# Kernel tuning notes

Hardware: AMD Instinct MI355X
Metric: run time of the kernel (lower is better)

The kernel has to match this reference:

```python
import jax, jax.numpy as jnp
import numpy as np

N = 65536      # total nodes = B * MAXN
E = 524288     # edges (avg degree 8)
DX = 32; DG = 32
IN_DIM = DX + 3 * DG   # 128, after concat(x, g0, g1, g2)
H = 256; OUT = 8; MAXN = 8192


def setup_inputs() -> dict:
    key = jax.random.key(0)
    ks = jax.random.split(key, 40)
    inp = {}
    inp['x'] = jax.random.normal(ks[0], (N, DX), jnp.float32)
    inp['g0'] = jax.random.normal(ks[1], (N, DG), jnp.float32)
    inp['g1'] = jax.random.normal(ks[2], (N, DG), jnp.float32)
    inp['g2'] = jax.random.normal(ks[3], (N, DG), jnp.float32)
    inp['edge_src'] = jax.random.randint(ks[4], (E,), 0, N, jnp.int32)
    inp['edge_dst'] = jax.random.randint(ks[5], (E,), 0, N, jnp.int32)
    dims = [(IN_DIM, H), (H, H), (H, H), (H, H)]
    k = 6
    for i, (di, do) in enumerate(dims):
        s = 1.0 / np.sqrt(di)
        inp[f'Wl{i}'] = jax.random.uniform(ks[k], (di, do), jnp.float32, -s, s); k += 1
        inp[f'Wr{i}'] = jax.random.uniform(ks[k], (di, do), jnp.float32, -s, s); k += 1
        inp[f'b{i}'] = jnp.zeros((do,), jnp.float32)
    s = 1.0 / np.sqrt(MAXN)
    inp['mlp1_W1'] = jax.random.uniform(ks[k], (MAXN, H), jnp.float32, -s, s); k += 1
    inp['mlp1_b1'] = jnp.zeros((H,), jnp.float32)
    s = 1.0 / np.sqrt(H)
    inp['mlp1_W2'] = jax.random.uniform(ks[k], (H, 1), jnp.float32, -s, s); k += 1
    inp['mlp1_b2'] = jnp.zeros((1,), jnp.float32)
    inp['bn_gamma'] = jnp.ones((H,), jnp.float32)
    inp['bn_beta'] = jnp.zeros((H,), jnp.float32)
    inp['mlp2_W1'] = jax.random.uniform(ks[k], (H, H), jnp.float32, -s, s); k += 1
    inp['mlp2_b1'] = jnp.zeros((H,), jnp.float32)
    inp['mlp2_W2'] = jax.random.uniform(ks[k], (H, OUT), jnp.float32, -s, s); k += 1
    inp['mlp2_b2'] = jnp.zeros((OUT,), jnp.float32)
    return inp


def _forward(x, g0, g1, g2, edge_src, edge_dst,
             Wl0, Wr0, b0, Wl1, Wr1, b1, Wl2, Wr2, b2, Wl3, Wr3, b3,
             mlp1_W1, mlp1_b1, mlp1_W2, mlp1_b2, bn_gamma, bn_beta,
             mlp2_W1, mlp2_b1, mlp2_W2, mlp2_b2):
    h = jnp.concatenate([x, g0, g1, g2], axis=1)  # [N, IN_DIM]
    # mean-aggregation denominator (in-degree, clamped at 1 like PyG mean)
    cnt = jnp.maximum(
        jax.ops.segment_sum(jnp.ones((E,), h.dtype), edge_dst, num_segments=N), 1.0)
    for Wl, Wr, b in ((Wl0, Wr0, b0), (Wl1, Wr1, b1), (Wl2, Wr2, b2), (Wl3, Wr3, b3)):
        agg = jax.ops.segment_sum(h[edge_src], edge_dst, num_segments=N) / cnt[:, None]
        # SAGEConv: lin_l(mean of neighbors) + lin_r(self) + bias, then ReLU
        h = jax.nn.relu(agg @ Wl + h @ Wr + b)
        # F.dropout in eval / deterministic reference: identity
    h = h.reshape(-1, H, MAXN)                               # [B, H, MAXN]
    h = jax.nn.relu(jnp.einsum('bhm,mk->bhk', h, mlp1_W1) + mlp1_b1)
    h = (jnp.einsum('bhk,ko->bho', h, mlp1_W2) + mlp1_b2)[..., 0]  # [B, H]
    mean = h.mean(axis=0)
    var = h.var(axis=0)
    h = (h - mean) / jnp.sqrt(var + 1e-5) * bn_gamma + bn_beta
    h = jax.nn.relu(h)
    h = jax.nn.relu(h @ mlp2_W1 + mlp2_b1)
    return h @ mlp2_W2 + mlp2_b2                              # [B, OUT]


def reference(x, g0, g1, g2, edge_src, edge_dst,
              Wl0, Wr0, b0, Wl1, Wr1, b1, Wl2, Wr2, b2, Wl3, Wr3, b3,
              mlp1_W1, mlp1_b1, mlp1_W2, mlp1_b2, bn_gamma, bn_beta,
              mlp2_W1, mlp2_b1, mlp2_W2, mlp2_b2):
    return _forward(x, g0, g1, g2, edge_src, edge_dst,
                    Wl0, Wr0, b0, Wl1, Wr1, b1, Wl2, Wr2, b2, Wl3, Wr3, b3,
                    mlp1_W1, mlp1_b1, mlp1_W2, mlp1_b2, bn_gamma, bn_beta,
                    mlp2_W1, mlp2_b1, mlp2_W2, mlp2_b2)
```

## Files before the change

### kernel.cpp

```cpp
#include <hip/hip_runtime.h>
#include <hip/hip_bf16.h>


#define NN 65536
#define EE 524288
#define ROWS 65537
#define PCSR_CAP 983040

using frag16 = __attribute__((ext_vector_type(8))) short;
using f32x4  = __attribute__((ext_vector_type(4))) float;
using us8    = __attribute__((ext_vector_type(8))) unsigned short;
using us4v   = __attribute__((ext_vector_type(4))) unsigned short;

__device__ __forceinline__ float b2f(unsigned short u) {
    union { unsigned u32; float f; } x; x.u32 = (unsigned)u << 16; return x.f;
}

__device__ __forceinline__ void gld_lds16(const void* g, void* l) {
    __builtin_amdgcn_global_load_lds(
        (const __attribute__((address_space(1))) void*)g,
        (__attribute__((address_space(3))) void*)l, 16, 0, 0);
}


__global__ void gs_zero_deg(int* deg) {
    int i = blockIdx.x * 256 + threadIdx.x;
    if (i < NN) deg[i] = 0;
}

__global__ void gs_hist(const int* __restrict__ dst, int* __restrict__ deg) {
    int e = blockIdx.x * 256 + threadIdx.x;
    atomicAdd(&deg[dst[e]], 1);
}

__global__ void gs_deg_reduce(const int* __restrict__ deg, int* __restrict__ bsum) {
    int t = threadIdx.x;
    int p = (deg[blockIdx.x * 256 + t] + 7) & ~7;
#pragma unroll
    for (int off = 32; off > 0; off >>= 1) p += __shfl_down(p, off);
    __shared__ int w4[4];
    if ((t & 63) == 0) w4[t >> 6] = p;
    __syncthreads();
    if (t == 0) bsum[blockIdx.x] = w4[0] + w4[1] + w4[2] + w4[3];
}

__global__ void gs_scan_bsum(const int* __restrict__ bsum, int* __restrict__ bofs,
                             int* __restrict__ prow) {
    __shared__ int part[256];
    int t = threadIdx.x;
    int v = bsum[t];
    part[t] = v;
    __syncthreads();
    for (int off = 1; off < 256; off <<= 1) {
        int add = (t >= off) ? part[t - off] : 0;
        __syncthreads();
        part[t] += add;
        __syncthreads();
    }
    bofs[t] = part[t] - v;
    if (t == 255) prow[NN] = part[255];
}

__global__ void gs_scan_apply(const int* __restrict__ deg, const int* __restrict__ bofs,
                              int* __restrict__ prow, int* __restrict__ cursor,
                              float* __restrict__ inv_cnt, int* __restrict__ pcsr,
                              __hip_bfloat16* __restrict__ P0,
                              __hip_bfloat16* __restrict__ P1) {
    __shared__ int part[256];
    int t = threadIdx.x;
    int i = blockIdx.x * 256 + t;
    int d = deg[i];
    int p = (d + 7) & ~7;
    part[t] = p;
    __syncthreads();
    for (int off = 1; off < 256; off <<= 1) {
        int add = (t >= off) ? part[t - off] : 0;
        __syncthreads();
        part[t] += add;
        __syncthreads();
    }
    int beg = bofs[blockIdx.x] + part[t] - p;
    prow[i] = beg;
    cursor[i] = beg;
    inv_cnt[i] = 1.0f / (float)(d > 0 ? d : 1);
    for (int j = d; j < p; ++j) pcsr[beg + j] = NN;
    if (blockIdx.x == 0) {
        ((unsigned*)(P0 + (size_t)NN * 512))[t] = 0u;
        ((unsigned*)(P1 + (size_t)NN * 512))[t] = 0u;
    }
}

__global__ void gs_bucket(const int* __restrict__ src, const int* __restrict__ dst,
                          int* __restrict__ cursor, int* __restrict__ pcsr) {
    int e = blockIdx.x * 256 + threadIdx.x;
    int d = dst[e];
    int p = atomicAdd(&cursor[d], 1);
    pcsr[p] = src[e];
}

struct TcvtArgs {
    const float* src[8];
    __hip_bfloat16* dst[8];
    int ldk[8];
    int kofs[8];
    int kblk[8];
};

__global__ void gs_tcvt_all(TcvtArgs a) {
    int z = blockIdx.z;
    if ((int)blockIdx.x >= a.kblk[z]) return;
    const float* src = a.src[z];
    __hip_bfloat16* dst = a.dst[z];
    int ldk = a.ldk[z], kofs = a.kofs[z];
    __shared__ float tile[32][33];
    int kb = blockIdx.x * 32, nb = blockIdx.y * 32;
    int tx = threadIdx.x, ty = threadIdx.y;
#pragma unroll
    for (int i = 0; i < 32; i += 8)
        tile[ty + i][tx] = src[(size_t)(kb + ty + i) * 256 + nb + tx];
    __syncthreads();
#pragma unroll
    for (int i = 0; i < 32; i += 8) {
        int n = nb + ty + i, k = kb + tx;
        dst[(size_t)n * ldk + kofs + k] = __float2bfloat16(tile[tx][ty + i]);
    }
}

__global__ void gs_tcvt(const float* __restrict__ src, __hip_bfloat16* __restrict__ dst,
                        int ldk, int kofs) {
    __shared__ float tile[32][33];
    int kb = blockIdx.x * 32, nb = blockIdx.y * 32;
    int tx = threadIdx.x, ty = threadIdx.y;
#pragma unroll
    for (int i = 0; i < 32; i += 8)
        tile[ty + i][tx] = src[(size_t)(kb + ty + i) * 256 + nb + tx];
    __syncthreads();
#pragma unroll
    for (int i = 0; i < 32; i += 8) {
        int n = nb + ty + i, k = kb + tx;
        dst[(size_t)n * ldk + kofs + k] = __float2bfloat16(tile[tx][ty + i]);
    }
}

__global__ void gs_concat_bf(const float* __restrict__ x, const float* __restrict__ g0,
                             const float* __restrict__ g1, const float* __restrict__ g2,
                             __hip_bfloat16* __restrict__ h) {
    int idx = blockIdx.x * 256 + threadIdx.x;
    int n = idx >> 5, q = idx & 31;
    int c0 = q * 4;
    const float* src = (c0 < 32) ? (x  + (size_t)n * 32 + c0)
                     : (c0 < 64) ? (g0 + (size_t)n * 32 + (c0 - 32))
                     : (c0 < 96) ? (g1 + (size_t)n * 32 + (c0 - 64))
                                 : (g2 + (size_t)n * 32 + (c0 - 96));
    f32x4 v = *(const f32x4*)src;
    union { us4v u; __hip_bfloat16 b[4]; } o;
#pragma unroll
    for (int r = 0; r < 4; ++r) o.b[r] = __float2bfloat16(v[r]);
    *(us4v*)(h + (size_t)n * 512 + 256 + c0) = o.u;
}

template <int DIM>
__global__ void gs_agg_bf(const __hip_bfloat16* __restrict__ hsrc,
                          __hip_bfloat16* __restrict__ adst,
                          const int* __restrict__ prow, const int* __restrict__ pcsr,
                          const float* __restrict__ inv_cnt) {
    constexpr int EL = DIM / 32;
    int wave = threadIdx.x >> 6;
    int lane = threadIdx.x & 63;
    int n = blockIdx.x * 4 + wave;
    int e = prow[n], pe = prow[n + 1];
    float iv = inv_cnt[n];
    const int half = lane >> 5;
    const __hip_bfloat16* base = hsrc + (lane & 31) * EL;
    float a[EL];
#pragma unroll
    for (int k = 0; k < EL; ++k) a[k] = 0.f;
    int4 sa, sb;
    if (e < pe) { sa = *(const int4*)(pcsr + e); sb = *(const int4*)(pcsr + e + 4); }
    while (e < pe) {
        int4 ca = sa, cb = sb;
        e += 8;
        if (e < pe) { sa = *(const int4*)(pcsr + e); sb = *(const int4*)(pcsr + e + 4); }
        int r0 = half ? ca.y : ca.x;
        int r1 = half ? ca.w : ca.z;
        int r2 = half ? cb.y : cb.x;
        int r3 = half ? cb.w : cb.z;
        if constexpr (DIM == 256) {
            us8 v0 = *(const us8*)(base + (size_t)r0 * 512);
            us8 v1 = *(const us8*)(base + (size_t)r1 * 512);
            us8 v2 = *(const us8*)(base + (size_t)r2 * 512);
            us8 v3 = *(const us8*)(base + (size_t)r3 * 512);
#pragma unroll
            for (int k = 0; k < 8; ++k)
                a[k] += b2f(v0[k]) + b2f(v1[k]) + b2f(v2[k]) + b2f(v3[k]);
        } else {
            us4v v0 = *(const us4v*)(base + (size_t)r0 * 512);
            us4v v1 = *(const us4v*)(base + (size_t)r1 * 512);
            us4v v2 = *(const us4v*)(base + (size_t)r2 * 512);
            us4v v3 = *(const us4v*)(base + (size_t)r3 * 512);
#pragma unroll
            for (int k = 0; k < 4; ++k)
                a[k] += b2f(v0[k]) + b2f(v1[k]) + b2f(v2[k]) + b2f(v3[k]);
        }
    }
#pragma unroll
    for (int k = 0; k < EL; ++k) a[k] += __shfl_xor(a[k], 32);
    if (half == 0) {
        union { us8 v8; us4v v4; __hip_bfloat16 b[8]; } o;
#pragma unroll
        for (int k = 0; k < EL; ++k) o.b[k] = __float2bfloat16(a[k] * iv);
        if constexpr (DIM == 256)
            *(us8*)(adst + (size_t)n * 512 + (lane & 31) * 8) = o.v8;
        else
            *(us4v*)(adst + (size_t)n * 512 + (lane & 31) * 4) = o.v4;
    }
}

__device__ __forceinline__ void mfma_block(const __hip_bfloat16* A, int lda,
                                           const __hip_bfloat16* Bt, int ldb,
                                           int kbeg, int kend, size_t row0, size_t nbase,
                                           __hip_bfloat16* As, __hip_bfloat16* Bs,
                                           f32x4 acc[4][4]) {
    const int t = threadIdx.x;
    const int lane = t & 63;
    const int w = t >> 6;
    const int wr = (w >> 1) * 64;
    const int wc = (w & 1) * 64;
    const int srow = w * 32 + (lane >> 3);
    const int scol = (lane & 7) * 8;
    for (int kc = kbeg; kc < kend; kc += 64) {
#pragma unroll
        for (int l = 0; l < 4; ++l) {
            gld_lds16(A + (row0 + srow + 8 * l) * (size_t)lda + kc + scol,
                      As + (w * 32 + 8 * l) * 64);
            gld_lds16(Bt + (nbase + srow + 8 * l) * (size_t)ldb + kc + scol,
                      Bs + (w * 32 + 8 * l) * 64);
        }
        __syncthreads();
#pragma unroll
        for (int kk = 0; kk < 64; kk += 32) {
            frag16 af[4], bf[4];
#pragma unroll
            for (int i = 0; i < 4; ++i)
                af[i] = *(const frag16*)(As + (wr + i * 16 + (lane & 15)) * 64 + kk + (lane >> 4) * 8);
#pragma unroll
            for (int j = 0; j < 4; ++j)
                bf[j] = *(const frag16*)(Bs + (wc + j * 16 + (lane & 15)) * 64 + kk + (lane >> 4) * 8);
#pragma unroll
            for (int i = 0; i < 4; ++i)
#pragma unroll
                for (int j = 0; j < 4; ++j)
                    acc[i][j] = __builtin_amdgcn_mfma_f32_16x16x32_bf16(bf[j], af[i], acc[i][j], 0, 0, 0);
        }
        __syncthreads();
    }
}

__global__ __launch_bounds__(256, 2)
void gs_gemm_bias_relu(const __hip_bfloat16* __restrict__ A, int lda, int K,
                       const __hip_bfloat16* __restrict__ Bt, int ldb,
                       const float* __restrict__ bias,
                       __hip_bfloat16* __restrict__ C, int ldc, int cofs) {
    __shared__ __hip_bfloat16 As[128 * 64];
    __shared__ __hip_bfloat16 Bs[128 * 64];
    f32x4 acc[4][4] = {};
    const size_t row0 = (size_t)blockIdx.x * 128;
    const size_t nbase = (size_t)blockIdx.y * 128;
    mfma_block(A, lda, Bt, ldb, 0, K, row0, nbase, As, Bs, acc);
    const int lane = threadIdx.x & 63;
    const int w = threadIdx.x >> 6;
    const int wr = (w >> 1) * 64, wc = (w & 1) * 64;
    const int nq = (lane >> 4) * 4;
    const int ml = lane & 15;
#pragma unroll
    for (int j = 0; j < 4; ++j) {
        int n0 = (int)nbase + wc + j * 16 + nq;
        f32x4 bv = *(const f32x4*)(bias + n0);
#pragma unroll
        for (int i = 0; i < 4; ++i) {
            size_t row = row0 + wr + i * 16 + ml;
            union { us4v v; __hip_bfloat16 b[4]; } o;
#pragma unroll
            for (int r = 0; r < 4; ++r)
                o.b[r] = __float2bfloat16(fmaxf(acc[i][j][r] + bv[r], 0.f));
            *(us4v*)(C + row * (size_t)ldc + cofs + n0) = o.v;
        }
    }
}

__global__ __launch_bounds__(256, 2)
void gs_gemm_splitk(const __hip_bfloat16* __restrict__ A, int lda,
                    const __hip_bfloat16* __restrict__ Bt, int ldb,
                    float* __restrict__ part) {
    __shared__ __hip_bfloat16 As[128 * 64];
    __shared__ __hip_bfloat16 Bs[128 * 64];
    f32x4 acc[4][4] = {};
    const size_t row0 = (size_t)blockIdx.x * 128;
    const size_t nbase = (size_t)blockIdx.y * 128;
    const int kbeg = blockIdx.z * 512;
    mfma_block(A, lda, Bt, ldb, kbeg, kbeg + 512, row0, nbase, As, Bs, acc);
    const int lane = threadIdx.x & 63;
    const int w = threadIdx.x >> 6;
    const int wr = (w >> 1) * 64, wc = (w & 1) * 64;
    const int nq = (lane >> 4) * 4;
    const int ml = lane & 15;
    float* p = part + (size_t)blockIdx.z * 2048 * 256;
#pragma unroll
    for (int j = 0; j < 4; ++j) {
        int n0 = (int)nbase + wc + j * 16 + nq;
#pragma unroll
        for (int i = 0; i < 4; ++i) {
            size_t row = row0 + wr + i * 16 + ml;
            *(f32x4*)(p + row * 256 + n0) = acc[i][j];
        }
    }
}

__global__ void gs_mlp1_pool(const float* __restrict__ part, const float* __restrict__ b1,
                             const float* __restrict__ W2, const float* __restrict__ b2,
                             float* __restrict__ pooled) {
    int r = blockIdx.x;
    int t = threadIdx.x;
    float s = 0.f;
#pragma unroll
    for (int ks = 0; ks < 16; ++ks) s += part[(size_t)ks * 524288 + r * 256 + t];
    s = fmaxf(s + b1[t], 0.f) * W2[t];
#pragma unroll
    for (int off = 32; off > 0; off >>= 1) s += __shfl_down(s, off);
    __shared__ float w4[4];
    if ((t & 63) == 0) w4[t >> 6] = s;
    __syncthreads();
    if (t == 0) pooled[r] = w4[0] + w4[1] + w4[2] + w4[3] + b2[0];
}

__global__ void gs_bn_mlp2(const float* __restrict__ pooled, const float* __restrict__ gamma,
                           const float* __restrict__ beta, const float* __restrict__ W1,
                           const float* __restrict__ b1, const float* __restrict__ W2,
                           const float* __restrict__ b2, float* __restrict__ out) {
    __shared__ float hb[8][256];
    __shared__ float h2[8][256];
    int t = threadIdx.x;
    {
        float v[8];
        float m = 0.f;
#pragma unroll
        for (int b = 0; b < 8; ++b) { v[b] = pooled[b * 256 + t]; m += v[b]; }
        m *= 0.125f;
        float var = 0.f;
#pragma unroll
        for (int b = 0; b < 8; ++b) { float d = v[b] - m; var += d * d; }
        var *= 0.125f;
        float is = 1.0f / sqrtf(var + 1e-5f);
        float g = gamma[t], bt = beta[t];
#pragma unroll
        for (int b = 0; b < 8; ++b) hb[b][t] = fmaxf((v[b] - m) * is * g + bt, 0.f);
    }
    __syncthreads();
    {
        float acc[8] = {};
        for (int i = 0; i < 256; ++i) {
            float w = W1[i * 256 + t];
#pragma unroll
            for (int b = 0; b < 8; ++b) acc[b] = fmaf(hb[b][i], w, acc[b]);
        }
        float bb = b1[t];
#pragma unroll
        for (int b = 0; b < 8; ++b) h2[b][t] = fmaxf(acc[b] + bb, 0.f);
    }
    __syncthreads();
    if (t < 64) {
        int b = t >> 3, o = t & 7;
        float acc = 0.f;
        for (int j = 0; j < 256; ++j) acc = fmaf(h2[b][j], W2[j * 8 + o], acc);
        out[b * 8 + o] = acc + b2[o];
    }
}

extern "C" void kernel_launch(void* const* d_in, const int* in_sizes, int n_in,
                              void* d_out, int out_size, void* d_ws, size_t ws_size,
                              hipStream_t stream) {
    const float* x  = (const float*)d_in[0];
    const float* g0 = (const float*)d_in[1];
    const float* g1 = (const float*)d_in[2];
    const float* g2 = (const float*)d_in[3];
    const int* edge_src = (const int*)d_in[4];
    const int* edge_dst = (const int*)d_in[5];
    const float* Wl[4] = {(const float*)d_in[6], (const float*)d_in[9],
                          (const float*)d_in[12], (const float*)d_in[15]};
    const float* Wr[4] = {(const float*)d_in[7], (const float*)d_in[10],
                          (const float*)d_in[13], (const float*)d_in[16]};
    const float* bs[4] = {(const float*)d_in[8], (const float*)d_in[11],
                          (const float*)d_in[14], (const float*)d_in[17]};
    const float* mlp1_W1 = (const float*)d_in[18];
    const float* mlp1_b1 = (const float*)d_in[19];
    const float* mlp1_W2 = (const float*)d_in[20];
    const float* mlp1_b2 = (const float*)d_in[21];
    const float* bn_gamma = (const float*)d_in[22];
    const float* bn_beta  = (const float*)d_in[23];
    const float* mlp2_W1 = (const float*)d_in[24];
    const float* mlp2_b1 = (const float*)d_in[25];
    const float* mlp2_W2 = (const float*)d_in[26];
    const float* mlp2_b2 = (const float*)d_in[27];
    float* out = (float*)d_out;

    char* ws = (char*)d_ws;
    __hip_bfloat16* P0 = (__hip_bfloat16*)ws;
    __hip_bfloat16* P1 = P0 + (size_t)ROWS * 512;
    __hip_bfloat16* WC0 = P1 + (size_t)ROWS * 512;
    __hip_bfloat16* WC1 = WC0 + 65536;
    __hip_bfloat16* WC2 = WC1 + 131072;
    __hip_bfloat16* WC3 = WC2 + 131072;
    __hip_bfloat16* W1T = WC3 + 131072;
    float* inv_cnt = (float*)(W1T + 2097152);
    int* ideg = (int*)(inv_cnt + 65536);
    int* prow = ideg + 65536;
    int* cursor = prow + 65544;
    int* bsum = cursor + 65536;
    int* bofs = bsum + 256;
    int* pcsr = bofs + 256;
    __hip_bfloat16* H4 = P0;
    float* pooled = (float*)P1 + 524288;
    float* PART = (float*)((char*)P1 + (size_t)(4 << 20));

    gs_zero_deg<<<256, 256, 0, stream>>>(ideg);
    gs_hist<<<EE / 256, 256, 0, stream>>>(edge_dst, ideg);
    gs_deg_reduce<<<256, 256, 0, stream>>>(ideg, bsum);
    gs_scan_bsum<<<1, 256, 0, stream>>>(bsum, bofs, prow);
    gs_scan_apply<<<256, 256, 0, stream>>>(ideg, bofs, prow, cursor, inv_cnt, pcsr, P0, P1);
    gs_bucket<<<EE / 256, 256, 0, stream>>>(edge_src, edge_dst, cursor, pcsr);

    {
        TcvtArgs a;
        const float* srcs[8] = {Wl[0], Wr[0], Wl[1], Wr[1], Wl[2], Wr[2], Wl[3], Wr[3]};
        __hip_bfloat16* dsts[8] = {WC0, WC0, WC1, WC1, WC2, WC2, WC3, WC3};
        int ldks[8] = {256, 256, 512, 512, 512, 512, 512, 512};
        int kofss[8] = {0, 128, 0, 256, 0, 256, 0, 256};
        int kblks[8] = {4, 4, 8, 8, 8, 8, 8, 8};
        for (int i = 0; i < 8; ++i) {
            a.src[i] = srcs[i]; a.dst[i] = dsts[i];
            a.ldk[i] = ldks[i]; a.kofs[i] = kofss[i]; a.kblk[i] = kblks[i];
        }
        gs_tcvt_all<<<dim3(8, 8, 8), dim3(32, 8), 0, stream>>>(a);
    }
    gs_tcvt<<<dim3(256, 8), dim3(32, 8), 0, stream>>>(mlp1_W1, W1T, 8192, 0);

    gs_concat_bf<<<NN * 32 / 256, 256, 0, stream>>>(x, g0, g1, g2, P0);

    gs_agg_bf<128><<<NN / 4, 256, 0, stream>>>(P0 + 256, P0 + 128, prow, pcsr, inv_cnt);
    gs_gemm_bias_relu<<<dim3(NN / 128, 2), 256, 0, stream>>>(P0 + 128, 512, 256, WC0, 256,
                                                             bs[0], P1, 512, 256);
    gs_agg_bf<256><<<NN / 4, 256, 0, stream>>>(P1 + 256, P1, prow, pcsr, inv_cnt);
    gs_gemm_bias_relu<<<dim3(NN / 128, 2), 256, 0, stream>>>(P1, 512, 512, WC1, 512,
                                                             bs[1], P0, 512, 256);
    gs_agg_bf<256><<<NN / 4, 256, 0, stream>>>(P0 + 256, P0, prow, pcsr, inv_cnt);
    gs_gemm_bias_relu<<<dim3(NN / 128, 2), 256, 0, stream>>>(P0, 512, 512, WC2, 512,
                                                             bs[2], P1, 512, 256);
    gs_agg_bf<256><<<NN / 4, 256, 0, stream>>>(P1 + 256, P1, prow, pcsr, inv_cnt);
    gs_gemm_bias_relu<<<dim3(NN / 128, 2), 256, 0, stream>>>(P1, 512, 512, WC3, 512,
                                                             bs[3], H4, 256, 0);

    gs_gemm_splitk<<<dim3(16, 2, 16), 256, 0, stream>>>(H4, 8192, W1T, 8192, PART);
    gs_mlp1_pool<<<2048, 256, 0, stream>>>(PART, mlp1_b1, mlp1_W2, mlp1_b2, pooled);

    gs_bn_mlp2<<<1, 256, 0, stream>>>(pooled, bn_gamma, bn_beta, mlp2_W1, mlp2_b1,
                                      mlp2_W2, mlp2_b2, out);
}
```

Measured before the change: 537.5 us.

## Use 256x256 double-buffered swizzled MFMA GEMM tiles with 8 waves

Replaces the 128x128 single-buffered GEMM with a 256-row by full-256-column tile computed by 8 waves per block. Global-to-LDS loads for the next K slice are issued before computing the current one, with XOR-swizzled LDS columns to avoid bank conflicts. Instruction priority is raised around the MFMA bursts. This targets LDS bank conflicts, load latency and redundant A reads across the two column blocks, at the cost of 128KB LDS per block, more accumulator registers and fewer blocks per launch.

Measured after the change: 524.7 us. 1.02x faster.

```diff
diff --git a/kernel.cpp b/kernel.cpp
--- a/kernel.cpp
+++ b/kernel.cpp
@@ -216,69 +216,92 @@
     }
 }
 
-__device__ __forceinline__ void mfma_block(const __hip_bfloat16* A, int lda,
-                                           const __hip_bfloat16* Bt, int ldb,
-                                           int kbeg, int kend, size_t row0, size_t nbase,
-                                           __hip_bfloat16* As, __hip_bfloat16* Bs,
-                                           f32x4 acc[4][4]) {
+
+__device__ __forceinline__ void stage_tile256(const __hip_bfloat16* __restrict__ A, int lda,
+                                              const __hip_bfloat16* __restrict__ Bt, int ldb,
+                                              size_t row0, int kc,
+                                              __hip_bfloat16* As, __hip_bfloat16* Bs) {
     const int t = threadIdx.x;
-    const int lane = t & 63;
-    const int w = t >> 6;
-    const int wr = (w >> 1) * 64;
-    const int wc = (w & 1) * 64;
-    const int srow = w * 32 + (lane >> 3);
-    const int scol = (lane & 7) * 8;
-    for (int kc = kbeg; kc < kend; kc += 64) {
-#pragma unroll
-        for (int l = 0; l < 4; ++l) {
-            gld_lds16(A + (row0 + srow + 8 * l) * (size_t)lda + kc + scol,
-                      As + (w * 32 + 8 * l) * 64);
-            gld_lds16(Bt + (nbase + srow + 8 * l) * (size_t)ldb + kc + scol,
-                      Bs + (w * 32 + 8 * l) * 64);
-        }
-        __syncthreads();
-#pragma unroll
-        for (int kk = 0; kk < 64; kk += 32) {
-            frag16 af[4], bf[4];
-#pragma unroll
-            for (int i = 0; i < 4; ++i)
-                af[i] = *(const frag16*)(As + (wr + i * 16 + (lane & 15)) * 64 + kk + (lane >> 4) * 8);
+#pragma unroll
+    for (int l = 0; l < 4; ++l) {
+        int c = l * 512 + t;
+        int row = c >> 3;
+        int col = ((c & 7) ^ (row & 7)) * 8;
+        gld_lds16(A + (row0 + row) * (size_t)lda + kc + col, As + c * 8);
+        gld_lds16(Bt + (size_t)row * ldb + kc + col, Bs + c * 8);
+    }
+}
+
+__device__ __forceinline__ void compute_tile256(const __hip_bfloat16* As,
+                                                const __hip_bfloat16* Bs,
+                                                int wm, int wn, int ml, int cq,
+                                                f32x4 (&acc)[8][4]) {
+#pragma unroll
+    for (int kk = 0; kk < 2; ++kk) {
+        const int g = kk * 4 + cq;
+        frag16 a[8], b[4];
+#pragma unroll
+        for (int i = 0; i < 8; ++i) {
+            int row = wm * 128 + i * 16 + ml;
+            a[i] = *(const frag16*)(As + row * 64 + ((g ^ (row & 7)) * 8));
+        }
+#pragma unroll
+        for (int j = 0; j < 4; ++j) {
+            int row = wn * 64 + j * 16 + ml;
+            b[j] = *(const frag16*)(Bs + row * 64 + ((g ^ (row & 7)) * 8));
+        }
+        __builtin_amdgcn_s_setprio(1);
+#pragma unroll
+        for (int i = 0; i < 8; ++i)
 #pragma unroll
             for (int j = 0; j < 4; ++j)
-                bf[j] = *(const frag16*)(Bs + (wc + j * 16 + (lane & 15)) * 64 + kk + (lane >> 4) * 8);
-#pragma unroll
-            for (int i = 0; i < 4; ++i)
-#pragma unroll
-                for (int j = 0; j < 4; ++j)
-                    acc[i][j] = __builtin_amdgcn_mfma_f32_16x16x32_bf16(bf[j], af[i], acc[i][j], 0, 0, 0);
-        }
-        __syncthreads();
-    }
-}
-
-__global__ __launch_bounds__(256, 2)
-void gs_gemm_bias_relu(const __hip_bfloat16* __restrict__ A, int lda, int K,
-                       const __hip_bfloat16* __restrict__ Bt, int ldb,
-                       const float* __restrict__ bias,
-                       __hip_bfloat16* __restrict__ C, int ldc, int cofs) {
-    __shared__ __hip_bfloat16 As[128 * 64];
-    __shared__ __hip_bfloat16 Bs[128 * 64];
-    f32x4 acc[4][4] = {};
-    const size_t row0 = (size_t)blockIdx.x * 128;
-    const size_t nbase = (size_t)blockIdx.y * 128;
-    mfma_block(A, lda, Bt, ldb, 0, K, row0, nbase, As, Bs, acc);
-    const int lane = threadIdx.x & 63;
-    const int w = threadIdx.x >> 6;
-    const int wr = (w >> 1) * 64, wc = (w & 1) * 64;
-    const int nq = (lane >> 4) * 4;
-    const int ml = lane & 15;
-#pragma unroll
-    for (int j = 0; j < 4; ++j) {
-        int n0 = (int)nbase + wc + j * 16 + nq;
-        f32x4 bv = *(const f32x4*)(bias + n0);
-#pragma unroll
-        for (int i = 0; i < 4; ++i) {
-            size_t row = row0 + wr + i * 16 + ml;
+                acc[i][j] = __builtin_amdgcn_mfma_f32_16x16x32_bf16(b[j], a[i], acc[i][j], 0, 0, 0);
+        __builtin_amdgcn_s_setprio(0);
+    }
+}
+
+__device__ __forceinline__ void gemm256_loop(const __hip_bfloat16* __restrict__ A, int lda,
+                                             const __hip_bfloat16* __restrict__ Bt, int ldb,
+                                             size_t row0, int kbeg, int nt,
+                                             __hip_bfloat16 (&As)[2][256 * 64],
+                                             __hip_bfloat16 (&Bs)[2][256 * 64],
+                                             int wm, int wn, int ml, int cq,
+                                             f32x4 (&acc)[8][4]) {
+    stage_tile256(A, lda, Bt, ldb, row0, kbeg, As[0], Bs[0]);
+    int cur = 0;
+    for (int kt = 0; kt < nt; ++kt) {
+        if (kt + 1 < nt) {
+            stage_tile256(A, lda, Bt, ldb, row0, kbeg + (kt + 1) * 64, As[cur ^ 1], Bs[cur ^ 1]);
+            asm volatile("s_waitcnt vmcnt(8)" ::: "memory");
+        } else {
+            asm volatile("s_waitcnt vmcnt(0)" ::: "memory");
+        }
+        asm volatile("s_barrier" ::: "memory");
+        compute_tile256(As[cur], Bs[cur], wm, wn, ml, cq, acc);
+        asm volatile("s_barrier" ::: "memory");
+        cur ^= 1;
+    }
+}
+
+__global__ __launch_bounds__(512, 2)
+void gs_gemm8_bias_relu(const __hip_bfloat16* __restrict__ A, int lda, int K,
+                        const __hip_bfloat16* __restrict__ Bt, int ldb,
+                        const float* __restrict__ bias,
+                        __hip_bfloat16* __restrict__ C, int ldc, int cofs) {
+    __shared__ __hip_bfloat16 As[2][256 * 64];
+    __shared__ __hip_bfloat16 Bs[2][256 * 64];
+    f32x4 acc[8][4] = {};
+    const size_t row0 = (size_t)blockIdx.x * 256;
+    const int lane = threadIdx.x & 63, wid = threadIdx.x >> 6;
+    const int wm = wid >> 2, wn = wid & 3, ml = lane & 15, cq = lane >> 4;
+    gemm256_loop(A, lda, Bt, ldb, row0, 0, K / 64, As, Bs, wm, wn, ml, cq, acc);
+#pragma unroll
+    for (int i = 0; i < 8; ++i) {
+        size_t row = row0 + wm * 128 + i * 16 + ml;
+#pragma unroll
+        for (int j = 0; j < 4; ++j) {
+            int n0 = wn * 64 + j * 16 + cq * 4;
+            f32x4 bv = *(const f32x4*)(bias + n0);
             union { us4v v; __hip_bfloat16 b[4]; } o;
 #pragma unroll
             for (int r = 0; r < 4; ++r)
@@ -288,29 +311,25 @@
     }
 }
 
-__global__ __launch_bounds__(256, 2)
-void gs_gemm_splitk(const __hip_bfloat16* __restrict__ A, int lda,
-                    const __hip_bfloat16* __restrict__ Bt, int ldb,
-                    float* __restrict__ part) {
-    __shared__ __hip_bfloat16 As[128 * 64];
-    __shared__ __hip_bfloat16 Bs[128 * 64];
-    f32x4 acc[4][4] = {};
-    const size_t row0 = (size_t)blockIdx.x * 128;
-    const size_t nbase = (size_t)blockIdx.y * 128;
-    const int kbeg = blockIdx.z * 512;
-    mfma_block(A, lda, Bt, ldb, kbeg, kbeg + 512, row0, nbase, As, Bs, acc);
-    const int lane = threadIdx.x & 63;
-    const int w = threadIdx.x >> 6;
-    const int wr = (w >> 1) * 64, wc = (w & 1) * 64;
-    const int nq = (lane >> 4) * 4;
-    const int ml = lane & 15;
-    float* p = part + (size_t)blockIdx.z * 2048 * 256;
-#pragma unroll
-    for (int j = 0; j < 4; ++j) {
-        int n0 = (int)nbase + wc + j * 16 + nq;
-#pragma unroll
-        for (int i = 0; i < 4; ++i) {
-            size_t row = row0 + wr + i * 16 + ml;
+__global__ __launch_bounds__(512, 2)
+void gs_gemm8_splitk(const __hip_bfloat16* __restrict__ A, int lda,
+                     const __hip_bfloat16* __restrict__ Bt, int ldb,
+                     float* __restrict__ part) {
+    __shared__ __hip_bfloat16 As[2][256 * 64];
+    __shared__ __hip_bfloat16 Bs[2][256 * 64];
+    f32x4 acc[8][4] = {};
+    const size_t row0 = (size_t)blockIdx.x * 256;
+    const int kbeg = blockIdx.y * 512;
+    const int lane = threadIdx.x & 63, wid = threadIdx.x >> 6;
+    const int wm = wid >> 2, wn = wid & 3, ml = lane & 15, cq = lane >> 4;
+    gemm256_loop(A, lda, Bt, ldb, row0, kbeg, 8, As, Bs, wm, wn, ml, cq, acc);
+    float* p = part + (size_t)blockIdx.y * 2048 * 256;
+#pragma unroll
+    for (int i = 0; i < 8; ++i) {
+        size_t row = row0 + wm * 128 + i * 16 + ml;
+#pragma unroll
+        for (int j = 0; j < 4; ++j) {
+            int n0 = wn * 64 + j * 16 + cq * 4;
             *(f32x4*)(p + row * 256 + n0) = acc[i][j];
         }
     }
@@ -447,19 +466,19 @@
     gs_concat_bf<<<NN * 32 / 256, 256, 0, stream>>>(x, g0, g1, g2, P0);
 
     gs_agg_bf<128><<<NN / 4, 256, 0, stream>>>(P0 + 256, P0 + 128, prow, pcsr, inv_cnt);
-    gs_gemm_bias_relu<<<dim3(NN / 128, 2), 256, 0, stream>>>(P0 + 128, 512, 256, WC0, 256,
-                                                             bs[0], P1, 512, 256);
+    gs_gemm8_bias_relu<<<NN / 256, 512, 0, stream>>>(P0 + 128, 512, 256, WC0, 256,
+                                                     bs[0], P1, 512, 256);
     gs_agg_bf<256><<<NN / 4, 256, 0, stream>>>(P1 + 256, P1, prow, pcsr, inv_cnt);
-    gs_gemm_bias_relu<<<dim3(NN / 128, 2), 256, 0, stream>>>(P1, 512, 512, WC1, 512,
-                                                             bs[1], P0, 512, 256);
+    gs_gemm8_bias_relu<<<NN / 256, 512, 0, stream>>>(P1, 512, 512, WC1, 512,
+                                                     bs[1], P0, 512, 256);
     gs_agg_bf<256><<<NN / 4, 256, 0, stream>>>(P0 + 256, P0, prow, pcsr, inv_cnt);
-    gs_gemm_bias_relu<<<dim3(NN / 128, 2), 256, 0, stream>>>(P0, 512, 512, WC2, 512,
-                                                             bs[2], P1, 512, 256);
+    gs_gemm8_bias_relu<<<NN / 256, 512, 0, stream>>>(P0, 512, 512, WC2, 512,
+                                                     bs[2], P1, 512, 256);
     gs_agg_bf<256><<<NN / 4, 256, 0, stream>>>(P1 + 256, P1, prow, pcsr, inv_cnt);
-    gs_gemm_bias_relu<<<dim3(NN / 128, 2), 256, 0, stream>>>(P1, 512, 512, WC3, 512,
-                                                             bs[3], H4, 256, 0);
-
-    gs_gemm_splitk<<<dim3(16, 2, 16), 256, 0, stream>>>(H4, 8192, W1T, 8192, PART);
+    gs_gemm8_bias_relu<<<NN / 256, 512, 0, stream>>>(P1, 512, 512, WC3, 512,
+                                                     bs[3], H4, 256, 0);
+
+    gs_gemm8_splitk<<<dim3(2048 / 256, 16), 512, 0, stream>>>(H4, 8192, W1T, 8192, PART);
     gs_mlp1_pool<<<2048, 256, 0, stream>>>(PART, mlp1_b1, mlp1_W2, mlp1_b2, pooled);
 
     gs_bn_mlp2<<<1, 256, 0, stream>>>(pooled, bn_gamma, bn_beta, mlp2_W1, mlp2_b1,
```
